# Performance work log

Measured on AMD Instinct MI355X. Metric: run time of the kernel, lower is better.

## Reference

```python
import jax, jax.numpy as jnp
import numpy as np

NEG_SLOPE = 0.2  # PyG GATConv default negative_slope


def _gat_dense(x, W, att_src, att_dst, bias):
    """PyG GATConv on a fully-connected graph (self-loops included) == dense attention.
    x: [N, F_in], W: [F_in, H*C], att_src/att_dst: [H, C], bias: [H*C] or [C].
    Returns per-head outputs [N, H, C] (bias added by caller after concat/mean).
    """
    H, C = att_src.shape
    N = x.shape[0]
    h = (x @ W).reshape(N, H, C)                      # transformed node feats
    s = jnp.einsum('nhc,hc->nh', h, att_src)          # alpha_src per source node
    t = jnp.einsum('nhc,hc->nh', h, att_dst)          # alpha_dst per dest node
    # e[i, j, h] = leaky_relu(alpha_dst[i] + alpha_src[j]); softmax over sources j
    e = jax.nn.leaky_relu(t[:, None, :] + s[None, :, :], NEG_SLOPE)  # [N, N, H]
    a = jax.nn.softmax(e, axis=1)
    out = jnp.einsum('ijh,jhc->ihc', a, h)            # aggregate sources -> dest
    return out


def setup_inputs() -> dict:
    key = jax.random.key(0)
    ks = jax.random.split(key, 11)
    N, D, C, H = 4096, 768, 128, 4
    sd1 = 1.0 / np.sqrt(D)
    sd2 = 1.0 / np.sqrt(H * C)
    sd3 = 1.0 / np.sqrt(C)
    return {
        'node_feats': jax.random.normal(ks[0], (N, D), dtype=jnp.float32),
        'W1': jax.random.normal(ks[1], (D, H * C), dtype=jnp.float32) * sd1,
        'att_src1': jax.random.normal(ks[2], (H, C), dtype=jnp.float32) * sd3,
        'att_dst1': jax.random.normal(ks[3], (H, C), dtype=jnp.float32) * sd3,
        'b1': jnp.zeros((H * C,), dtype=jnp.float32),
        'W2': jax.random.normal(ks[4], (H * C, C), dtype=jnp.float32) * sd2,
        'att_src2': jax.random.normal(ks[5], (1, C), dtype=jnp.float32) * sd3,
        'att_dst2': jax.random.normal(ks[6], (1, C), dtype=jnp.float32) * sd3,
        'b2': jnp.zeros((C,), dtype=jnp.float32),
        'fcW': jax.random.normal(ks[7], (C, D), dtype=jnp.float32) * sd3,
        'fcb': jnp.zeros((D,), dtype=jnp.float32),
    }


def reference(node_feats, W1, att_src1, att_dst1, b1, W2, att_src2, att_dst2, b2, fcW, fcb):
    N = node_feats.shape[0]
    # GAT layer 1: 4 heads, concat=True
    x = _gat_dense(node_feats, W1, att_src1, att_dst1, b1).reshape(N, -1) + b1
    x = jax.nn.elu(x)
    # GAT layer 2: 1 head, concat=False (mean over the single head == identity)
    x = _gat_dense(x, W2, att_src2, att_dst2, b2)[:, 0, :] + b2
    x = jax.nn.elu(x)
    x = x.mean(axis=0)            # [gat_hidden]
    return x @ fcW + fcb          # [hidden_dim]
```

## Files before the change

kernel.cpp:

```cpp
#include <hip/hip_runtime.h>
#include <hip/hip_bf16.h>


#define NNODE 4096
#define CDIM 128
#define TW 132
#define NEG 0.2f
#define CHUNK 64
#define NCHUNK 64
#define SEG 8
#define SEGK (NNODE / SEG)

typedef __bf16 bf16x8 __attribute__((ext_vector_type(8)));
typedef float f32x4 __attribute__((ext_vector_type(4)));

__device__ __forceinline__ unsigned short f2b(float f) {
  unsigned int u = __float_as_uint(f);
  u += 0x7fffu + ((u >> 16) & 1u);
  return (unsigned short)(u >> 16);
}

__global__ __launch_bounds__(256) void prep_kernel(const float* __restrict__ x,
                                                   const float* __restrict__ W1,
                                                   const float* __restrict__ W2,
                                                   unsigned short* __restrict__ xb,
                                                   unsigned short* __restrict__ W1t,
                                                   unsigned short* __restrict__ W2t) {
  __shared__ float tile[64][65];
  int b = blockIdx.x, t = threadIdx.x;
  if (b < 3072) {
    int i = b * 256 + t;
    float4 v = ((const float4*)x)[i];
    ushort4 o;
    o.x = f2b(v.x); o.y = f2b(v.y); o.z = f2b(v.z); o.w = f2b(v.w);
    ((ushort4*)xb)[i] = o;
    return;
  }
  const float* W; unsigned short* Wt; int K, N, n0, k0;
  if (b < 3072 + 96) {
    int b2 = b - 3072; W = W1; Wt = W1t; K = 768; N = 512;
    n0 = (b2 & 7) * 64; k0 = (b2 >> 3) * 64;
  } else {
    int b3 = b - 3072 - 96; W = W2; Wt = W2t; K = 512; N = 128;
    n0 = (b3 & 1) * 64; k0 = (b3 >> 1) * 64;
  }
  for (int p = 0; p < 16; p++) {
    int e = p * 256 + t;
    int rr = e >> 6, cc = e & 63;
    tile[rr][cc] = W[(size_t)(k0 + rr) * N + n0 + cc];
  }
  __syncthreads();
  for (int p = 0; p < 16; p++) {
    int e = p * 256 + t;
    int rr = e >> 6, cc = e & 63;
    Wt[(size_t)(n0 + rr) * K + k0 + cc] = f2b(tile[cc][rr]);
  }
}

template <int BM, int BN>
__global__ __launch_bounds__(256) void mfma_gemm_bt(const unsigned short* __restrict__ A,
                                                    const unsigned short* __restrict__ Bt,
                                                    float* __restrict__ C,
                                                    int M, int N, int K) {
  __shared__ __align__(16) unsigned short As[BM * 40];
  __shared__ __align__(16) unsigned short Bs[BN * 40];
  constexpr int WM = BM / 2, WN = BN / 2;
  constexpr int FI = WM / 16, FJ = WN / 16;
  constexpr int EA = BM * 32 / 8;
  constexpr int EB = BN * 32 / 8;
  constexpr int NA = (EA + 255) / 256;
  constexpr int NB = (EB + 255) / 256;
  int tid = threadIdx.x;
  int lane = tid & 63, wave = tid >> 6;
  int wm = (wave >> 1) * WM, wn = (wave & 1) * WN;
  int m0 = blockIdx.y * BM, n0 = blockIdx.x * BN;
  int fm = lane & 15, fq = lane >> 4;
  f32x4 acc[FI][FJ] = {};
  uint4 ar[NA], br[NB];
#pragma unroll
  for (int q = 0; q < NA; q++) {
    int e = q * 256 + tid;
    if (e < EA) {
      int r = e >> 2, kk = (e & 3) * 8;
      ar[q] = *(const uint4*)(A + (size_t)(m0 + r) * K + kk);
    }
  }
#pragma unroll
  for (int q = 0; q < NB; q++) {
    int e = q * 256 + tid;
    if (e < EB) {
      int r = e >> 2, kk = (e & 3) * 8;
      br[q] = *(const uint4*)(Bt + (size_t)(n0 + r) * K + kk);
    }
  }
  for (int k0 = 0; k0 < K; k0 += 32) {
    __syncthreads();
#pragma unroll
    for (int q = 0; q < NA; q++) {
      int e = q * 256 + tid;
      if (e < EA) {
        int r = e >> 2, kk = (e & 3) * 8;
        *(uint4*)&As[r * 40 + kk] = ar[q];
      }
    }
#pragma unroll
    for (int q = 0; q < NB; q++) {
      int e = q * 256 + tid;
      if (e < EB) {
        int r = e >> 2, kk = (e & 3) * 8;
        *(uint4*)&Bs[r * 40 + kk] = br[q];
      }
    }
    __syncthreads();
    if (k0 + 32 < K) {
#pragma unroll
      for (int q = 0; q < NA; q++) {
        int e = q * 256 + tid;
        if (e < EA) {
          int r = e >> 2, kk = (e & 3) * 8;
          ar[q] = *(const uint4*)(A + (size_t)(m0 + r) * K + k0 + 32 + kk);
        }
      }
#pragma unroll
      for (int q = 0; q < NB; q++) {
        int e = q * 256 + tid;
        if (e < EB) {
          int r = e >> 2, kk = (e & 3) * 8;
          br[q] = *(const uint4*)(Bt + (size_t)(n0 + r) * K + k0 + 32 + kk);
        }
      }
    }
    bf16x8 af[FI], bfr[FJ];
#pragma unroll
    for (int i = 0; i < FI; i++)
      af[i] = *(const bf16x8*)&As[(wm + i * 16 + fm) * 40 + fq * 8];
#pragma unroll
    for (int j = 0; j < FJ; j++)
      bfr[j] = *(const bf16x8*)&Bs[(wn + j * 16 + fm) * 40 + fq * 8];
#pragma unroll
    for (int i = 0; i < FI; i++)
#pragma unroll
      for (int j = 0; j < FJ; j++)
        acc[i][j] = __builtin_amdgcn_mfma_f32_16x16x32_bf16(af[i], bfr[j], acc[i][j], 0, 0, 0);
  }
#pragma unroll
  for (int i = 0; i < FI; i++) {
#pragma unroll
    for (int j = 0; j < FJ; j++) {
      int r = m0 + wm + i * 16 + fq * 4;
      int ccol = n0 + wn + j * 16 + fm;
#pragma unroll
      for (int reg = 0; reg < 4; reg++)
        C[(size_t)(r + reg) * N + ccol] = acc[i][j][reg];
    }
  }
}

__global__ void st_kernel(const float* __restrict__ h,
                          const float* __restrict__ asrc,
                          const float* __restrict__ adst,
                          float* __restrict__ s, float* __restrict__ t, int H) {
  int n = blockIdx.x;
  int wave = threadIdx.x >> 6, lane = threadIdx.x & 63;
  int HC = H * CDIM;
  float2 hv = *(const float2*)&h[(size_t)n * HC + wave * CDIM + lane * 2];
  float2 av = *(const float2*)&asrc[wave * CDIM + lane * 2];
  float2 dv = *(const float2*)&adst[wave * CDIM + lane * 2];
  float ps = hv.x * av.x + hv.y * av.y;
  float pt = hv.x * dv.x + hv.y * dv.y;
#pragma unroll
  for (int o = 32; o > 0; o >>= 1) {
    ps += __shfl_down(ps, o, 64);
    pt += __shfl_down(pt, o, 64);
  }
  if (lane == 0) {
    s[(size_t)wave * NNODE + n] = ps;
    t[(size_t)wave * NNODE + n] = pt;
  }
}

__global__ __launch_bounds__(256) void rank_count_kernel(const float* __restrict__ s,
                                                         int* __restrict__ partial) {
  __shared__ __align__(16) float keys[SEGK];
  int hh = blockIdx.z, seg = blockIdx.y, tid = threadIdx.x;
  const float* sp = s + (size_t)hh * NNODE;
  for (int k = tid; k < SEGK; k += 256) keys[k] = sp[seg * SEGK + k];
  __syncthreads();
  int mi = blockIdx.x * 256 + tid;
  float mk = sp[mi];
  int jbase = seg * SEGK;
  int cnt = 0;
#pragma unroll 4
  for (int j = 0; j < SEGK; j += 4) {
    float4 kv = *(const float4*)&keys[j];
    int jj = jbase + j;
    cnt += (kv.x < mk) || (kv.x == mk && (jj + 0) < mi);
    cnt += (kv.y < mk) || (kv.y == mk && (jj + 1) < mi);
    cnt += (kv.z < mk) || (kv.z == mk && (jj + 2) < mi);
    cnt += (kv.w < mk) || (kv.w == mk && (jj + 3) < mi);
  }
  partial[((size_t)hh * SEG + seg) * NNODE + mi] = cnt;
}

__global__ __launch_bounds__(256) void rank_scatter_kernel(const float* __restrict__ s,
                                                           const int* __restrict__ partial,
                                                           float* __restrict__ ss,
                                                           int* __restrict__ si) {
  int hh = blockIdx.y;
  int mi = blockIdx.x * 256 + threadIdx.x;
  int rank = 0;
#pragma unroll
  for (int g = 0; g < SEG; g++) rank += partial[((size_t)hh * SEG + g) * NNODE + mi];
  ss[(size_t)hh * NNODE + rank] = s[(size_t)hh * NNODE + mi];
  si[(size_t)hh * NNODE + rank] = mi;
}

__global__ __launch_bounds__(128) void passA_kernel(const float* __restrict__ h,
                                                    const float* __restrict__ ss,
                                                    const int* __restrict__ si,
                                                    float* __restrict__ partP,
                                                    float* __restrict__ partM, int H) {
  __shared__ float eP[CHUNK], eM[CHUNK];
  __shared__ int ids[CHUNK];
  int b = blockIdx.x, hh = b / NCHUNK, ci = b % NCHUNK;
  int c = threadIdx.x;
  int HC = H * CDIM;
  int base = ci * CHUNK;
  if (c < CHUNK) {
    float sv = ss[(size_t)hh * NNODE + base + c];
    ids[c] = si[(size_t)hh * NNODE + base + c];
    eP[c] = expf(sv);
    eM[c] = expf(NEG * sv);
  }
  __syncthreads();
  float sp = 0.f, sm = 0.f;
  for (int kb = 0; kb < CHUNK; kb += 8) {
    float v[8];
#pragma unroll
    for (int j = 0; j < 8; j++)
      v[j] = h[(size_t)ids[kb + j] * HC + hh * CDIM + c];
#pragma unroll
    for (int j = 0; j < 8; j++) {
      sp = fmaf(eP[kb + j], v[j], sp);
      sm = fmaf(eM[kb + j], v[j], sm);
    }
  }
  size_t o = ((size_t)hh * NCHUNK + ci) * TW;
  partP[o + c] = sp;
  partM[o + c] = sm;
  if (c == 0) {
    float zp = 0.f, zm = 0.f;
#pragma unroll
    for (int k = 0; k < CHUNK; k++) { zp += eP[k]; zm += eM[k]; }
    partP[o + 128] = zp;
    partM[o + 128] = zm;
  }
}

__global__ __launch_bounds__(128) void passC_kernel(const float* __restrict__ h,
                                                    const float* __restrict__ ss,
                                                    const int* __restrict__ si,
                                                    const float* __restrict__ partP,
                                                    const float* __restrict__ partM,
                                                    float* __restrict__ SS,
                                                    float* __restrict__ PP, int H) {
  __shared__ float hrow[CHUNK][CDIM];
  __shared__ float eP[CHUNK], eM[CHUNK];
  __shared__ int ids[CHUNK];
  int b = blockIdx.x, hh = b / NCHUNK, ci = b % NCHUNK;
  int c = threadIdx.x;
  int HC = H * CDIM;
  int base = ci * CHUNK;
  size_t hb = (size_t)hh * (NNODE + 1);
  if (c < CHUNK) {
    float sv = ss[(size_t)hh * NNODE + base + c];
    ids[c] = si[(size_t)hh * NNODE + base + c];
    eP[c] = expf(sv);
    eM[c] = expf(NEG * sv);
  }
  __syncthreads();
  float cm = 0.f, cp = 0.f;
  for (int g0 = 0; g0 < NCHUNK; g0 += 16) {
    float vm[16], vp[16];
#pragma unroll
    for (int j = 0; j < 16; j++) {
      size_t o = ((size_t)hh * NCHUNK + g0 + j) * TW + c;
      vm[j] = partM[o];
      vp[j] = partP[o];
    }
#pragma unroll
    for (int j = 0; j < 16; j++) {
      if (g0 + j < ci) cm += vm[j];
      if (g0 + j > ci) cp += vp[j];
    }
  }
  float zcm = 0.f, zcp = 0.f;
  if (c == 0) {
    for (int g0 = 0; g0 < NCHUNK; g0 += 16) {
      float vm[16], vp[16];
#pragma unroll
      for (int j = 0; j < 16; j++) {
        size_t o = ((size_t)hh * NCHUNK + g0 + j) * TW + 128;
        vm[j] = partM[o];
        vp[j] = partP[o];
      }
#pragma unroll
      for (int j = 0; j < 16; j++) {
        if (g0 + j < ci) zcm += vm[j];
        if (g0 + j > ci) zcp += vp[j];
      }
    }
  }
  for (int kb = 0; kb < CHUNK; kb += 8) {
    float v[8];
#pragma unroll
    for (int j = 0; j < 8; j++)
      v[j] = h[(size_t)ids[kb + j] * HC + hh * CDIM + c];
#pragma unroll
    for (int j = 0; j < 8; j++) hrow[kb + j][c] = v[j];
  }
  float runm = cm, runzm = zcm;
#pragma unroll 8
  for (int k = 0; k < CHUNK; k++) {
    size_t row = (hb + base + k) * TW;
    PP[row + c] = runm;
    if (c == 0) PP[row + 128] = runzm;
    runm = fmaf(eM[k], hrow[k][c], runm);
    runzm += eM[k];
  }
  if (ci == NCHUNK - 1) {
    size_t row = (hb + NNODE) * TW;
    PP[row + c] = runm;
    if (c == 0) PP[row + 128] = runzm;
  }
  float runp = cp, runzp = zcp;
#pragma unroll 8
  for (int k = CHUNK - 1; k >= 0; k--) {
    runp = fmaf(eP[k], hrow[k][c], runp);
    runzp += eP[k];
    size_t row = (hb + base + k) * TW;
    SS[row + c] = runp;
    if (c == 0) SS[row + 128] = runzp;
  }
  if (ci == NCHUNK - 1) {
    size_t row = (hb + NNODE) * TW;
    SS[row + c] = 0.f;
    if (c == 0) SS[row + 128] = 0.f;
  }
}

template <typename OUT>
__global__ __launch_bounds__(128) void attend_kernel(const float* __restrict__ SS,
                                                     const float* __restrict__ PP,
                                                     const float* __restrict__ ss,
                                                     const float* __restrict__ tt,
                                                     const float* __restrict__ bias,
                                                     OUT* __restrict__ out, int H) {
  int b = blockIdx.x;
  int n = b / H, hh = b % H;
  int c = threadIdx.x;
  float tv = tt[(size_t)hh * NNODE + n];
  const float* sp = ss + (size_t)hh * NNODE;
  float thr = -tv;
  int lo = 0, hi = NNODE;
  while (lo < hi) { int mid = (lo + hi) >> 1; if (sp[mid] < thr) lo = mid + 1; else hi = mid; }
  size_t hb = (size_t)hh * (NNODE + 1);
  float wp = expf(tv), wm = expf(NEG * tv);
  float num = wp * SS[(hb + lo) * TW + c] + wm * PP[(hb + lo) * TW + c];
  float Z = wp * SS[(hb + lo) * TW + 128] + wm * PP[(hb + lo) * TW + 128];
  float o = num / Z + bias[hh * CDIM + c];
  float r = (o > 0.f) ? o : (expf(o) - 1.f);
  if constexpr (sizeof(OUT) == 2)
    out[(size_t)n * (H * CDIM) + hh * CDIM + c] = f2b(r);
  else
    out[(size_t)n * (H * CDIM) + hh * CDIM + c] = r;
}

__global__ __launch_bounds__(256) void mean_kernel(const float* __restrict__ x,
                                                   float* __restrict__ m) {
  __shared__ float red[256];
  int c = blockIdx.x, tid = threadIdx.x;
  float acc = 0.f;
  for (int i = tid; i < NNODE; i += 256) acc += x[(size_t)i * CDIM + c];
  red[tid] = acc; __syncthreads();
  for (int o = 128; o > 0; o >>= 1) { if (tid < o) red[tid] += red[tid + o]; __syncthreads(); }
  if (tid == 0) m[c] = red[0] * (1.f / NNODE);
}

__global__ __launch_bounds__(256) void fc_kernel(const float* __restrict__ m,
                                                 const float* __restrict__ fcW,
                                                 const float* __restrict__ fcb,
                                                 float* __restrict__ out) {
  int d = blockIdx.x * 256 + threadIdx.x;
  float acc = fcb[d];
  for (int c2 = 0; c2 < CDIM; c2++) acc = fmaf(m[c2], fcW[c2 * 768 + d], acc);
  out[d] = acc;
}

extern "C" void kernel_launch(void* const* d_in, const int* in_sizes, int n_in,
                              void* d_out, int out_size, void* d_ws, size_t ws_size,
                              hipStream_t stream) {
  const float* x   = (const float*)d_in[0];
  const float* W1  = (const float*)d_in[1];
  const float* as1 = (const float*)d_in[2];
  const float* ad1 = (const float*)d_in[3];
  const float* b1  = (const float*)d_in[4];
  const float* W2  = (const float*)d_in[5];
  const float* as2 = (const float*)d_in[6];
  const float* ad2 = (const float*)d_in[7];
  const float* b2  = (const float*)d_in[8];
  const float* fcW = (const float*)d_in[9];
  const float* fcb = (const float*)d_in[10];

  float* ws = (float*)d_ws;
  size_t off = 0;
  auto alloc = [&](size_t nfloats) { float* p = ws + off; off += nfloats; return p; };

  float* h1  = alloc((size_t)NNODE * 512);
  float* x2f = alloc((size_t)NNODE * 256 + 64 + 16384);
  float* h2  = alloc((size_t)NNODE * 128);
  float* x3  = alloc((size_t)NNODE * 128);
  float* s1  = alloc((size_t)4 * NNODE);
  float* t1  = alloc((size_t)4 * NNODE);
  float* sS1 = alloc((size_t)4 * NNODE);
  int*   sI1 = (int*)alloc((size_t)4 * NNODE);
  float* SS1 = alloc((size_t)4 * (NNODE + 1) * TW);
  float* PP1 = alloc((size_t)4 * (NNODE + 1) * TW);
  float* pP1 = alloc((size_t)4 * NCHUNK * TW);
  float* pM1 = alloc((size_t)4 * NCHUNK * TW);
  float* s2  = alloc(NNODE);
  float* t2  = alloc(NNODE);
  float* sS2 = alloc(NNODE);
  int*   sI2 = (int*)alloc(NNODE);
  float* SS2 = alloc((size_t)(NNODE + 1) * TW);
  float* PP2 = alloc((size_t)(NNODE + 1) * TW);
  float* pP2 = alloc((size_t)NCHUNK * TW);
  float* pM2 = alloc((size_t)NCHUNK * TW);
  float* mv  = alloc(128);
  int*   rparts = (int*)alloc((size_t)4 * SEG * NNODE);

  unsigned short* xb  = (unsigned short*)PP1;
  unsigned short* W1t = (unsigned short*)SS1;
  unsigned short* x2b = (unsigned short*)x2f;
  unsigned short* W2t = (unsigned short*)(x2f + NNODE * 256 + 64);

  prep_kernel<<<3072 + 96 + 16, 256, 0, stream>>>(x, W1, W2, xb, W1t, W2t);
  mfma_gemm_bt<64, 64><<<dim3(512 / 64, NNODE / 64), 256, 0, stream>>>(xb, W1t, h1, NNODE, 512, 768);
  st_kernel<<<NNODE, 4 * 64, 0, stream>>>(h1, as1, ad1, s1, t1, 4);
  rank_count_kernel<<<dim3(NNODE / 256, SEG, 4), 256, 0, stream>>>(s1, rparts);
  rank_scatter_kernel<<<dim3(NNODE / 256, 4), 256, 0, stream>>>(s1, rparts, sS1, sI1);
  passA_kernel<<<4 * NCHUNK, 128, 0, stream>>>(h1, sS1, sI1, pP1, pM1, 4);
  passC_kernel<<<4 * NCHUNK, 128, 0, stream>>>(h1, sS1, sI1, pP1, pM1, SS1, PP1, 4);
  attend_kernel<unsigned short><<<NNODE * 4, 128, 0, stream>>>(SS1, PP1, sS1, t1, b1, x2b, 4);
  mfma_gemm_bt<32, 64><<<dim3(128 / 64, NNODE / 32), 256, 0, stream>>>(x2b, W2t, h2, NNODE, 128, 512);
  st_kernel<<<NNODE, 1 * 64, 0, stream>>>(h2, as2, ad2, s2, t2, 1);
  rank_count_kernel<<<dim3(NNODE / 256, SEG, 1), 256, 0, stream>>>(s2, rparts);
  rank_scatter_kernel<<<dim3(NNODE / 256, 1), 256, 0, stream>>>(s2, rparts, sS2, sI2);
  passA_kernel<<<NCHUNK, 128, 0, stream>>>(h2, sS2, sI2, pP2, pM2, 1);
  passC_kernel<<<NCHUNK, 128, 0, stream>>>(h2, sS2, sI2, pP2, pM2, SS2, PP2, 1);
  attend_kernel<float><<<NNODE, 128, 0, stream>>>(SS2, PP2, sS2, t2, b2, x3, 1);
  mean_kernel<<<128, 256, 0, stream>>>(x3, mv);
  fc_kernel<<<3, 256, 0, stream>>>(mv, fcW, fcb, (float*)d_out);
}
```

Measured before the change: 224.9 us.

## Fuse attention-score dot products into GEMM epilogue and column mean into attend

Removes the two st_kernel launches by computing the per-node source/destination attention logits in the MFMA GEMM epilogue, reducing across lanes with shuffles and accumulating with atomics into buffers that prep_kernel now zeroes. The attend kernel processes several (node, head) items per 256-thread block, and for layer 2 it accumulates column sums with atomics, so mean_kernel is dropped and fc_kernel applies the 1/N scale. The intent is to cut launch count and the re-read of h; the cost is float atomics, which make the summation order nondeterministic, and a reordered workspace layout so one contiguous zero-fill covers s1, t1, s2, t2 and mv.

Result: slower. 233.2 us (+3.7%).

```diff
diff --git a/kernel.cpp b/kernel.cpp
--- a/kernel.cpp
+++ b/kernel.cpp
@@ -25,7 +25,8 @@
                                                    const float* __restrict__ W2,
                                                    unsigned short* __restrict__ xb,
                                                    unsigned short* __restrict__ W1t,
-                                                   unsigned short* __restrict__ W2t) {
+                                                   unsigned short* __restrict__ W2t,
+                                                   float* __restrict__ zbase) {
   __shared__ float tile[64][65];
   int b = blockIdx.x, t = threadIdx.x;
   if (b < 3072) {
@@ -36,6 +37,14 @@
     ((ushort4*)xb)[i] = o;
     return;
   }
+  if (b >= 3072 + 96 + 16) {
+    int idx = (b - 3072 - 96 - 16) * 256 + t;
+    if (idx < 10272) {
+      float4 z = {0.f, 0.f, 0.f, 0.f};
+      ((float4*)zbase)[idx] = z;
+    }
+    return;
+  }
   const float* W; unsigned short* Wt; int K, N, n0, k0;
   if (b < 3072 + 96) {
     int b2 = b - 3072; W = W1; Wt = W1t; K = 768; N = 512;
@@ -61,6 +70,10 @@
 __global__ __launch_bounds__(256) void mfma_gemm_bt(const unsigned short* __restrict__ A,
                                                     const unsigned short* __restrict__ Bt,
                                                     float* __restrict__ C,
+                                                    const float* __restrict__ asrc,
+                                                    const float* __restrict__ adst,
+                                                    float* __restrict__ s,
+                                                    float* __restrict__ t,
                                                     int M, int N, int K) {
   __shared__ __align__(16) unsigned short As[BM * 40];
   __shared__ __align__(16) unsigned short Bs[BN * 40];
@@ -154,28 +167,35 @@
         C[(size_t)(r + reg) * N + ccol] = acc[i][j][reg];
     }
   }
-}
-
-__global__ void st_kernel(const float* __restrict__ h,
-                          const float* __restrict__ asrc,
-                          const float* __restrict__ adst,
-                          float* __restrict__ s, float* __restrict__ t, int H) {
-  int n = blockIdx.x;
-  int wave = threadIdx.x >> 6, lane = threadIdx.x & 63;
-  int HC = H * CDIM;
-  float2 hv = *(const float2*)&h[(size_t)n * HC + wave * CDIM + lane * 2];
-  float2 av = *(const float2*)&asrc[wave * CDIM + lane * 2];
-  float2 dv = *(const float2*)&adst[wave * CDIM + lane * 2];
-  float ps = hv.x * av.x + hv.y * av.y;
-  float pt = hv.x * dv.x + hv.y * dv.y;
-#pragma unroll
-  for (int o = 32; o > 0; o >>= 1) {
-    ps += __shfl_down(ps, o, 64);
-    pt += __shfl_down(pt, o, 64);
-  }
-  if (lane == 0) {
-    s[(size_t)wave * NNODE + n] = ps;
-    t[(size_t)wave * NNODE + n] = pt;
+  int hh = (n0 + wn) / CDIM;
+  float av[FJ], dv[FJ];
+#pragma unroll
+  for (int j = 0; j < FJ; j++) {
+    int col = (n0 + wn + j * 16 + fm) & (CDIM - 1);
+    av[j] = asrc[hh * CDIM + col];
+    dv[j] = adst[hh * CDIM + col];
+  }
+#pragma unroll
+  for (int i = 0; i < FI; i++) {
+#pragma unroll
+    for (int reg = 0; reg < 4; reg++) {
+      float ssum = 0.f, tsum = 0.f;
+#pragma unroll
+      for (int j = 0; j < FJ; j++) {
+        ssum = fmaf(acc[i][j][reg], av[j], ssum);
+        tsum = fmaf(acc[i][j][reg], dv[j], tsum);
+      }
+#pragma unroll
+      for (int o = 1; o < 16; o <<= 1) {
+        ssum += __shfl_xor(ssum, o, 64);
+        tsum += __shfl_xor(tsum, o, 64);
+      }
+      if (fm == 0) {
+        int r = m0 + wm + i * 16 + fq * 4 + reg;
+        atomicAdd(&s[(size_t)hh * NNODE + r], ssum);
+        atomicAdd(&t[(size_t)hh * NNODE + r], tsum);
+      }
+    }
   }
 }
 
@@ -349,51 +369,54 @@
   }
 }
 
-template <typename OUT>
-__global__ __launch_bounds__(128) void attend_kernel(const float* __restrict__ SS,
+template <typename OUT, int IPB, bool COLSUM>
+__global__ __launch_bounds__(256) void attend_kernel(const float* __restrict__ SS,
                                                      const float* __restrict__ PP,
                                                      const float* __restrict__ ss,
                                                      const float* __restrict__ tt,
                                                      const float* __restrict__ bias,
-                                                     OUT* __restrict__ out, int H) {
-  int b = blockIdx.x;
-  int n = b / H, hh = b % H;
-  int c = threadIdx.x;
-  float tv = tt[(size_t)hh * NNODE + n];
-  const float* sp = ss + (size_t)hh * NNODE;
-  float thr = -tv;
-  int lo = 0, hi = NNODE;
-  while (lo < hi) { int mid = (lo + hi) >> 1; if (sp[mid] < thr) lo = mid + 1; else hi = mid; }
-  size_t hb = (size_t)hh * (NNODE + 1);
-  float wp = expf(tv), wm = expf(NEG * tv);
-  float num = wp * SS[(hb + lo) * TW + c] + wm * PP[(hb + lo) * TW + c];
-  float Z = wp * SS[(hb + lo) * TW + 128] + wm * PP[(hb + lo) * TW + 128];
-  float o = num / Z + bias[hh * CDIM + c];
-  float r = (o > 0.f) ? o : (expf(o) - 1.f);
-  if constexpr (sizeof(OUT) == 2)
-    out[(size_t)n * (H * CDIM) + hh * CDIM + c] = f2b(r);
-  else
-    out[(size_t)n * (H * CDIM) + hh * CDIM + c] = r;
-}
-
-__global__ __launch_bounds__(256) void mean_kernel(const float* __restrict__ x,
-                                                   float* __restrict__ m) {
+                                                     OUT* __restrict__ out,
+                                                     float* __restrict__ colsum, int H) {
   __shared__ float red[256];
-  int c = blockIdx.x, tid = threadIdx.x;
-  float acc = 0.f;
-  for (int i = tid; i < NNODE; i += 256) acc += x[(size_t)i * CDIM + c];
-  red[tid] = acc; __syncthreads();
-  for (int o = 128; o > 0; o >>= 1) { if (tid < o) red[tid] += red[tid + o]; __syncthreads(); }
-  if (tid == 0) m[c] = red[0] * (1.f / NNODE);
-}
-
-__global__ __launch_bounds__(256) void fc_kernel(const float* __restrict__ m,
+  int half = threadIdx.x >> 7, c = threadIdx.x & 127;
+  int base = blockIdx.x * IPB;
+  float csum = 0.f;
+#pragma unroll
+  for (int q = 0; q < IPB / 2; q++) {
+    int b = base + q * 2 + half;
+    int n = b / H, hh = b % H;
+    float tv = tt[(size_t)hh * NNODE + n];
+    const float* sp = ss + (size_t)hh * NNODE;
+    float thr = -tv;
+    int lo = 0, hi = NNODE;
+    while (lo < hi) { int mid = (lo + hi) >> 1; if (sp[mid] < thr) lo = mid + 1; else hi = mid; }
+    size_t hb = (size_t)hh * (NNODE + 1);
+    float wp = expf(tv), wm = expf(NEG * tv);
+    float num = wp * SS[(hb + lo) * TW + c] + wm * PP[(hb + lo) * TW + c];
+    float Z = wp * SS[(hb + lo) * TW + 128] + wm * PP[(hb + lo) * TW + 128];
+    float o = num / Z + bias[hh * CDIM + c];
+    float r = (o > 0.f) ? o : (expf(o) - 1.f);
+    if constexpr (sizeof(OUT) == 2)
+      out[(size_t)n * (H * CDIM) + hh * CDIM + c] = f2b(r);
+    else
+      out[(size_t)n * (H * CDIM) + hh * CDIM + c] = r;
+    if constexpr (COLSUM) csum += r;
+  }
+  if constexpr (COLSUM) {
+    red[threadIdx.x] = csum;
+    __syncthreads();
+    if (threadIdx.x < 128) atomicAdd(&colsum[c], red[threadIdx.x] + red[threadIdx.x + 128]);
+  }
+}
+
+__global__ __launch_bounds__(256) void fc_kernel(const float* __restrict__ colsum,
                                                  const float* __restrict__ fcW,
                                                  const float* __restrict__ fcb,
                                                  float* __restrict__ out) {
   int d = blockIdx.x * 256 + threadIdx.x;
   float acc = fcb[d];
-  for (int c2 = 0; c2 < CDIM; c2++) acc = fmaf(m[c2], fcW[c2 * 768 + d], acc);
+  const float invN = 1.f / NNODE;
+  for (int c2 = 0; c2 < CDIM; c2++) acc = fmaf(colsum[c2] * invN, fcW[c2 * 768 + d], acc);
   out[d] = acc;
 }
 
@@ -422,21 +445,21 @@
   float* x3  = alloc((size_t)NNODE * 128);
   float* s1  = alloc((size_t)4 * NNODE);
   float* t1  = alloc((size_t)4 * NNODE);
+  float* s2  = alloc(NNODE);
+  float* t2  = alloc(NNODE);
+  float* mv  = alloc(128);
   float* sS1 = alloc((size_t)4 * NNODE);
   int*   sI1 = (int*)alloc((size_t)4 * NNODE);
   float* SS1 = alloc((size_t)4 * (NNODE + 1) * TW);
   float* PP1 = alloc((size_t)4 * (NNODE + 1) * TW);
   float* pP1 = alloc((size_t)4 * NCHUNK * TW);
   float* pM1 = alloc((size_t)4 * NCHUNK * TW);
-  float* s2  = alloc(NNODE);
-  float* t2  = alloc(NNODE);
   float* sS2 = alloc(NNODE);
   int*   sI2 = (int*)alloc(NNODE);
   float* SS2 = alloc((size_t)(NNODE + 1) * TW);
   float* PP2 = alloc((size_t)(NNODE + 1) * TW);
   float* pP2 = alloc((size_t)NCHUNK * TW);
   float* pM2 = alloc((size_t)NCHUNK * TW);
-  float* mv  = alloc(128);
   int*   rparts = (int*)alloc((size_t)4 * SEG * NNODE);
 
   unsigned short* xb  = (unsigned short*)PP1;
@@ -444,21 +467,22 @@
   unsigned short* x2b = (unsigned short*)x2f;
   unsigned short* W2t = (unsigned short*)(x2f + NNODE * 256 + 64);
 
-  prep_kernel<<<3072 + 96 + 16, 256, 0, stream>>>(x, W1, W2, xb, W1t, W2t);
-  mfma_gemm_bt<64, 64><<<dim3(512 / 64, NNODE / 64), 256, 0, stream>>>(xb, W1t, h1, NNODE, 512, 768);
-  st_kernel<<<NNODE, 4 * 64, 0, stream>>>(h1, as1, ad1, s1, t1, 4);
+  prep_kernel<<<3072 + 96 + 16 + 41, 256, 0, stream>>>(x, W1, W2, xb, W1t, W2t, s1);
+  mfma_gemm_bt<64, 64><<<dim3(512 / 64, NNODE / 64), 256, 0, stream>>>(
+      xb, W1t, h1, as1, ad1, s1, t1, NNODE, 512, 768);
   rank_count_kernel<<<dim3(NNODE / 256, SEG, 4), 256, 0, stream>>>(s1, rparts);
   rank_scatter_kernel<<<dim3(NNODE / 256, 4), 256, 0, stream>>>(s1, rparts, sS1, sI1);
   passA_kernel<<<4 * NCHUNK, 128, 0, stream>>>(h1, sS1, sI1, pP1, pM1, 4);
   passC_kernel<<<4 * NCHUNK, 128, 0, stream>>>(h1, sS1, sI1, pP1, pM1, SS1, PP1, 4);
-  attend_kernel<unsigned short><<<NNODE * 4, 128, 0, stream>>>(SS1, PP1, sS1, t1, b1, x2b, 4);
-  mfma_gemm_bt<32, 64><<<dim3(128 / 64, NNODE / 32), 256, 0, stream>>>(x2b, W2t, h2, NNODE, 128, 512);
-  st_kernel<<<NNODE, 1 * 64, 0, stream>>>(h2, as2, ad2, s2, t2, 1);
+  attend_kernel<unsigned short, 4, false><<<NNODE * 4 / 4, 256, 0, stream>>>(
+      SS1, PP1, sS1, t1, b1, x2b, nullptr, 4);
+  mfma_gemm_bt<32, 64><<<dim3(128 / 64, NNODE / 32), 256, 0, stream>>>(
+      x2b, W2t, h2, as2, ad2, s2, t2, NNODE, 128, 512);
   rank_count_kernel<<<dim3(NNODE / 256, SEG, 1), 256, 0, stream>>>(s2, rparts);
   rank_scatter_kernel<<<dim3(NNODE / 256, 1), 256, 0, stream>>>(s2, rparts, sS2, sI2);
   passA_kernel<<<NCHUNK, 128, 0, stream>>>(h2, sS2, sI2, pP2, pM2, 1);
   passC_kernel<<<NCHUNK, 128, 0, stream>>>(h2, sS2, sI2, pP2, pM2, SS2, PP2, 1);
-  attend_kernel<float><<<NNODE, 128, 0, stream>>>(SS2, PP2, sS2, t2, b2, x3, 1);
-  mean_kernel<<<128, 256, 0, stream>>>(x3, mv);
+  attend_kernel<float, 8, true><<<NNODE / 8, 256, 0, stream>>>(
+      SS2, PP2, sS2, t2, b2, x3, mv, 1);
   fc_kernel<<<3, 256, 0, stream>>>(mv, fcW, fcb, (float*)d_out);
 }
```
